# Optimization experiments

Hardware: AMD Instinct MI355X
Metric: run time of the kernel (lower is better)

The kernel has to match this reference:

```python
import jax, jax.numpy as jnp
import numpy as np

B, N = 4, 4096
CIN, COUT = 64, 64
K, R, BOX = 3, 32, 4
MLP = COUT * 4
HEADS = 4
EPS = 0.0


def setup_inputs() -> dict:
    key = jax.random.key(0)
    ks = jax.random.split(key, 16)
    s = lambda i, shape: jax.random.normal(ks[i], shape, jnp.float32) * 0.05
    return dict(
        features=jax.random.normal(ks[0], (B, CIN, N), jnp.float32),
        coords=jax.random.normal(ks[1], (B, 3, N), jnp.float32),
        conv_w=s(2, (COUT, CIN, K, K, K)), conv_b=jnp.zeros((COUT,), jnp.float32),
        ln1_g=jnp.ones((COUT,), jnp.float32), ln1_b=jnp.zeros((COUT,), jnp.float32),
        qkv_w=s(3, (3 * COUT, COUT)), qkv_b=jnp.zeros((3 * COUT,), jnp.float32),
        proj_w=s(4, (COUT, COUT)), proj_b=jnp.zeros((COUT,), jnp.float32),
        ln2_g=jnp.ones((COUT,), jnp.float32), ln2_b=jnp.zeros((COUT,), jnp.float32),
        mlp_w1=s(5, (MLP, COUT)), mlp_b1=jnp.zeros((MLP,), jnp.float32),
        mlp_w2=s(6, (COUT, MLP)), mlp_b2=jnp.zeros((COUT,), jnp.float32),
        se_w1=s(7, (COUT // 8, COUT)), se_w2=s(8, (COUT, COUT // 8)),
        pt_in_w=s(9, (COUT, CIN)), pt_in_b=jnp.zeros((COUT,), jnp.float32),
        q_w=s(10, (COUT // 4, COUT)), k_w=s(11, (COUT // 4, COUT)),
        v_w=s(12, (COUT, COUT)),
        trans_w=s(13, (COUT, COUT)), trans_b=jnp.zeros((COUT,), jnp.float32),
    )


def layernorm(x, g, b):
    m = x.mean(-1, keepdims=True)
    v = x.var(-1, keepdims=True)
    return (x - m) * jax.lax.rsqrt(v + 1e-5) * g + b


def voxelize(features, coords):
    # PVCNN-style: center, normalize to [0,1], scale to [0, R-1]; scatter-mean.
    c = coords - coords.mean(axis=2, keepdims=True)  # (B,3,N)
    mx = jnp.sqrt((c ** 2).sum(axis=1, keepdims=True)).max(axis=2, keepdims=True)
    nc = c / (2.0 * mx + EPS) + 0.5
    nc = jnp.clip(nc * R, 0.0, R - 1)  # float coords in [0, R-1]
    vc = jnp.round(nc).astype(jnp.int32)
    idx = (vc[:, 0] * R + vc[:, 1]) * R + vc[:, 2]
    idx = (idx + jnp.arange(B, dtype=jnp.int32)[:, None] * R ** 3).reshape(-1)
    flat = features.transpose(0, 2, 1).reshape(B * N, CIN)
    sums = jax.ops.segment_sum(flat, idx, num_segments=B * R ** 3)
    cnt = jax.ops.segment_sum(jnp.ones((B * N,), jnp.float32), idx, num_segments=B * R ** 3)
    avg = sums / jnp.maximum(cnt, 1.0)[:, None]
    grid = avg.reshape(B, R, R, R, CIN).transpose(0, 4, 1, 2, 3)  # (B,C,R,R,R)
    return grid, nc


def devoxelize(grid, nc):
    # trilinear gather from (B,C,R,R,R) at float coords nc (B,3,N)
    g = grid.reshape(B, COUT, R ** 3)
    x0 = jnp.floor(nc)
    f = nc - x0
    x0 = x0.astype(jnp.int32)
    out = jnp.zeros((B, COUT, N), jnp.float32)
    for dx in (0, 1):
        for dy in (0, 1):
            for dz in (0, 1):
                xi = jnp.clip(x0[:, 0] + dx, 0, R - 1)
                yi = jnp.clip(x0[:, 1] + dy, 0, R - 1)
                zi = jnp.clip(x0[:, 2] + dz, 0, R - 1)
                idx = (xi * R + yi) * R + zi  # (B,N)
                w = ((f[:, 0] if dx else 1 - f[:, 0]) *
                     (f[:, 1] if dy else 1 - f[:, 1]) *
                     (f[:, 2] if dz else 1 - f[:, 2]))
                vals = jnp.take_along_axis(g, jnp.broadcast_to(idx[:, None, :], (B, COUT, N)), axis=2)
                out = out + vals * w[:, None, :]
    return out


def voxel_encoder(grid, conv_w, conv_b, ln1_g, ln1_b, qkv_w, qkv_b, proj_w, proj_b,
                  ln2_g, ln2_b, mlp_w1, mlp_b1, mlp_w2, mlp_b2):
    x = jax.lax.conv_general_dilated(grid, conv_w, (1, 1, 1), 'SAME',
                                     dimension_numbers=('NCDHW', 'OIDHW', 'NCDHW'))
    x = jax.nn.relu(x + conv_b[None, :, None, None, None])
    nb = R // BOX
    # window partition -> (B*nb^3, BOX^3, C)
    t = x.transpose(0, 2, 3, 4, 1).reshape(B, nb, BOX, nb, BOX, nb, BOX, COUT)
    t = t.transpose(0, 1, 3, 5, 2, 4, 6, 7).reshape(B * nb ** 3, BOX ** 3, COUT)
    h = layernorm(t, ln1_g, ln1_b)
    qkv = h @ qkv_w.T + qkv_b
    q, k, v = jnp.split(qkv, 3, axis=-1)
    hd = COUT // HEADS
    sh = lambda z: z.reshape(z.shape[0], z.shape[1], HEADS, hd).transpose(0, 2, 1, 3)
    q, k, v = sh(q), sh(k), sh(v)
    attn = jax.nn.softmax(jnp.einsum('whid,whjd->whij', q, k) / np.float32(np.sqrt(hd)), axis=-1)
    o = jnp.einsum('whij,whjd->whid', attn, v).transpose(0, 2, 1, 3).reshape(t.shape)
    t = t + (o @ proj_w.T + proj_b)
    h = layernorm(t, ln2_g, ln2_b)
    t = t + (jax.nn.gelu(h @ mlp_w1.T + mlp_b1) @ mlp_w2.T + mlp_b2)
    t = t.reshape(B, nb, nb, nb, BOX, BOX, BOX, COUT)
    t = t.transpose(0, 1, 4, 2, 5, 3, 6, 7).reshape(B, R, R, R, COUT)
    return t.transpose(0, 4, 1, 2, 3)


def se3d(x, w1, w2):
    s = x.mean(axis=(2, 3, 4))  # (B,C)
    s = jax.nn.sigmoid(jax.nn.relu(s @ w1.T) @ w2.T)
    return x * s[:, :, None, None, None]


def point_branch(features, pt_in_w, pt_in_b, q_w, k_w, v_w, trans_w, trans_b):
    # PCT-style offset self-attention over points (shared transformer)
    x = jax.nn.relu(jnp.einsum('oc,bcn->bon', pt_in_w, features) + pt_in_b[None, :, None])
    q = jnp.einsum('dc,bcn->bdn', q_w, x)
    k = jnp.einsum('dc,bcn->bdn', k_w, x)
    v = jnp.einsum('oc,bcn->bon', v_w, x)
    attn = jax.nn.softmax(jnp.einsum('bdn,bdm->bnm', q, k) / np.float32(np.sqrt(q.shape[1])), axis=-1)
    o = jnp.einsum('bom,bnm->bon', v, attn)
    off = jax.nn.relu(jnp.einsum('oc,bcn->bon', trans_w, x - o) + trans_b[None, :, None])
    return x + off


def reference(features, coords, conv_w, conv_b, ln1_g, ln1_b, qkv_w, qkv_b, proj_w, proj_b,
              ln2_g, ln2_b, mlp_w1, mlp_b1, mlp_w2, mlp_b2, se_w1, se_w2,
              pt_in_w, pt_in_b, q_w, k_w, v_w, trans_w, trans_b):
    grid, nc = voxelize(features, coords)
    vf = voxel_encoder(grid, conv_w, conv_b, ln1_g, ln1_b, qkv_w, qkv_b, proj_w, proj_b,
                       ln2_g, ln2_b, mlp_w1, mlp_b1, mlp_w2, mlp_b2)
    vf = se3d(vf, se_w1, se_w2)
    vf = devoxelize(vf, nc)
    fused = vf + point_branch(features, pt_in_w, pt_in_b, q_w, k_w, v_w, trans_w, trans_b)
    return fused, coords
```

## Files before the change

kernel.cpp:

```cpp
#include <hip/hip_runtime.h>

#define BN 4
#define NP 4096
#define RV 32
#define VX (RV*RV*RV)

typedef __attribute__((ext_vector_type(8))) short bf16x8;
typedef __attribute__((ext_vector_type(4))) float f32x4;

__device__ __forceinline__ float bf2f(unsigned short u){
  union{unsigned u;float f;}v; v.u=((unsigned)u)<<16; return v.f; }
__device__ __forceinline__ unsigned short f2bf(float f){
  union{float f;unsigned u;}v; v.f=f; unsigned r=v.u + 0x7fffu + ((v.u>>16)&1u);
  return (unsigned short)(r>>16); }
__device__ __forceinline__ float2 bfp2f2(unsigned p){
  union{unsigned u;float f;}a,b; a.u=p<<16; b.u=p&0xffff0000u;
  float2 r; r.x=a.f; r.y=b.f; return r; }
__device__ __forceinline__ unsigned pack2bf(float a, float b){
  return (unsigned)f2bf(a) | ((unsigned)f2bf(b) << 16); }

union ABu { uint4 u; bf16x8 v; };

__global__ void stats_kernel(const float* __restrict__ coords, float* __restrict__ stats)
{
  __shared__ float red[256];
  __shared__ float mean[3];
  const int b = blockIdx.x;
  const int tid = threadIdx.x;
  float s0=0.f,s1=0.f,s2=0.f;
  for (int n = tid; n < NP; n += 256) {
    s0 += coords[((size_t)(b*3)+0)*NP + n];
    s1 += coords[((size_t)(b*3)+1)*NP + n];
    s2 += coords[((size_t)(b*3)+2)*NP + n];
  }
  float sv[3] = {s0,s1,s2};
  for (int ax = 0; ax < 3; ax++) {
    __syncthreads();
    red[tid] = sv[ax];
    __syncthreads();
    for (int st = 128; st > 0; st >>= 1) {
      if (tid < st) red[tid] += red[tid + st];
      __syncthreads();
    }
    if (tid == 0) mean[ax] = red[0] * (1.f / NP);
  }
  __syncthreads();
  float mx = 0.f;
  for (int n = tid; n < NP; n += 256) {
    float d0 = coords[((size_t)(b*3)+0)*NP + n] - mean[0];
    float d1 = coords[((size_t)(b*3)+1)*NP + n] - mean[1];
    float d2 = coords[((size_t)(b*3)+2)*NP + n] - mean[2];
    mx = fmaxf(mx, sqrtf(d0*d0 + d1*d1 + d2*d2));
  }
  __syncthreads();
  red[tid] = mx;
  __syncthreads();
  for (int st = 128; st > 0; st >>= 1) {
    if (tid < st) red[tid] = fmaxf(red[tid], red[tid + st]);
    __syncthreads();
  }
  if (tid == 0) {
    stats[b*4+0] = mean[0]; stats[b*4+1] = mean[1];
    stats[b*4+2] = mean[2]; stats[b*4+3] = red[0];
  }
}

__global__ void scatter_kernel(const float* __restrict__ features,
                               const float* __restrict__ coords,
                               const float* __restrict__ stats,
                               float* __restrict__ nc,
                               float* __restrict__ sums, float* __restrict__ cnt)
{
  int t = blockIdx.x*256 + threadIdx.x;
  int part = t & 3;
  int p = t >> 2;
  int b = p >> 12;
  int n = p & 4095;
  float m0 = stats[b*4+0], m1 = stats[b*4+1], m2 = stats[b*4+2], mx = stats[b*4+3];
  float inv = 1.f / (2.f * mx);
  float c0 = (coords[((size_t)(b*3)+0)*NP + n] - m0) * inv + 0.5f;
  float c1 = (coords[((size_t)(b*3)+1)*NP + n] - m1) * inv + 0.5f;
  float c2 = (coords[((size_t)(b*3)+2)*NP + n] - m2) * inv + 0.5f;
  float g0 = fminf(fmaxf(c0 * 32.f, 0.f), 31.f);
  float g1 = fminf(fmaxf(c1 * 32.f, 0.f), 31.f);
  float g2 = fminf(fmaxf(c2 * 32.f, 0.f), 31.f);
  int v0 = (int)rintf(g0), v1 = (int)rintf(g1), v2 = (int)rintf(g2);
  int idx = (v0*32 + v1)*32 + v2 + b*VX;
  if (part == 0) {
    nc[((size_t)(b*3)+0)*NP + n] = g0;
    nc[((size_t)(b*3)+1)*NP + n] = g1;
    nc[((size_t)(b*3)+2)*NP + n] = g2;
    atomicAdd(&cnt[idx], 1.f);
  }
  const float* fp = features + (size_t)(b*64)*NP + n;
  float* sp = sums + (size_t)idx*64;
  for (int i = part*16; i < part*16+16; i++)
    atomicAdd(&sp[i], fp[(size_t)i*NP]);
}

__global__ void wprep_kernel(const float* __restrict__ wt, unsigned short* __restrict__ wpre)
{
  int t = blockIdx.x*256 + threadIdx.x;
  if (t >= 27*64*8) return;
  int c16 = t & 7, o = (t >> 3) & 63, tap = t >> 9;
  size_t dst = ((size_t)(tap*64 + o)*8 + (c16 ^ (o & 7))) * 8;
  #pragma unroll
  for (int j = 0; j < 8; j++) {
    int i = c16*8 + j;
    wpre[dst + j] = f2bf(wt[(o*64 + i)*27 + tap]);
  }
}

__global__ void eprep_kernel(const float* __restrict__ qkv_w, const float* __restrict__ proj_w,
                             const float* __restrict__ w1, const float* __restrict__ w2,
                             const float* __restrict__ pt_in_w, const float* __restrict__ q_w,
                             const float* __restrict__ k_w, const float* __restrict__ v_w,
                             unsigned short* __restrict__ dst)
{
  int t = blockIdx.x*256 + threadIdx.x;
  if (t >= 59392) return;
  float v;
  if (t < 4096)       v = qkv_w[t] * 0.25f;
  else if (t < 12288) v = qkv_w[t];
  else if (t < 16384) v = proj_w[t-12288];
  else if (t < 32768) v = w1[t-16384];
  else if (t < 49152) v = w2[t-32768];
  else {
    int t2 = t - 49152;
    if (t2 < 4096)      v = pt_in_w[t2];
    else if (t2 < 5120) v = q_w[t2-4096] * 0.25f;
    else if (t2 < 6144) v = k_w[t2-5120];
    else                v = v_w[t2-6144];
  }
  dst[t] = f2bf(v);
}

__global__ __launch_bounds__(256) void conv_mfma_kernel(
    const float* __restrict__ sums, const float* __restrict__ cnt,
    const unsigned short* __restrict__ wpre,
    const float* __restrict__ bias, unsigned short* __restrict__ gout)
{
  __shared__ uint4 plane[6*34*8];
  __shared__ uint4 wsm[3*64*8];
  const int tid = threadIdx.x;
  const int blk = blockIdx.x;
  const int yq = blk & 7, z = (blk >> 3) & 31, b = blk >> 8;
  const int y0 = yq * 4;
  const int w  = tid >> 6;
  const int lm = tid & 15;
  const int kg = (tid >> 4) & 3;

  f32x4 acc[2][4];
  #pragma unroll
  for (int mt = 0; mt < 2; mt++)
    #pragma unroll
    for (int nt = 0; nt < 4; nt++)
      #pragma unroll
      for (int r = 0; r < 4; r++) acc[mt][nt][r] = 0.f;

  float bv[4];
  #pragma unroll
  for (int nt = 0; nt < 4; nt++) bv[nt] = bias[nt*16 + lm];

  for (int kd = 0; kd < 3; kd++) {
    const int zz = z + kd - 1;
    if (zz < 0 || zz >= 32) continue;
    __syncthreads();
    for (int e = tid; e < 6*34*8; e += 256) {
      int c16 = e & 7;
      int sx  = (e >> 3) % 34;
      int yl  = e / (34*8);
      int yy = y0 - 1 + yl, x = sx - 1;
      uint4 val = make_uint4(0u,0u,0u,0u);
      if (yy >= 0 && yy < 32 && x >= 0 && x < 32) {
        size_t vox = (size_t)(b*VX) + (zz*32 + yy)*32 + x;
        float rc = 1.f / fmaxf(cnt[vox], 1.f);
        const float* src = sums + vox*64 + c16*8;
        float4 f0 = *(const float4*)(src);
        float4 f1 = *(const float4*)(src + 4);
        val.x = pack2bf(f0.x*rc, f0.y*rc);
        val.y = pack2bf(f0.z*rc, f0.w*rc);
        val.z = pack2bf(f1.x*rc, f1.y*rc);
        val.w = pack2bf(f1.z*rc, f1.w*rc);
      }
      plane[(yl*34 + sx)*8 + (c16 ^ (sx & 7))] = val;
    }
    for (int kh = 0; kh < 3; kh++) {
      __syncthreads();
      const uint4* wsrc = (const uint4*)wpre + (size_t)((kd*3 + kh)*3)*512;
      for (int e = tid; e < 1536; e += 256) wsm[e] = wsrc[e];
      __syncthreads();
      const int yi = w + kh;
      #pragma unroll
      for (int kw = 0; kw < 3; kw++) {
        const int sxa = lm + kw, sxb = sxa + 16;
        const int swz = sxa & 7;
        #pragma unroll
        for (int ch = 0; ch < 2; ch++) {
          const int cb = ch*4 + kg;
          ABu a0, a1, w0, w1, w2, w3;
          a0.u = plane[(yi*34 + sxa)*8 + (cb ^ swz)];
          a1.u = plane[(yi*34 + sxb)*8 + (cb ^ swz)];
          const int wsz = cb ^ (lm & 7);
          w0.u = wsm[(kw*64 +      lm)*8 + wsz];
          w1.u = wsm[(kw*64 + 16 + lm)*8 + wsz];
          w2.u = wsm[(kw*64 + 32 + lm)*8 + wsz];
          w3.u = wsm[(kw*64 + 48 + lm)*8 + wsz];
          acc[0][0] = __builtin_amdgcn_mfma_f32_16x16x32_bf16(a0.v, w0.v, acc[0][0], 0,0,0);
          acc[1][0] = __builtin_amdgcn_mfma_f32_16x16x32_bf16(a1.v, w0.v, acc[1][0], 0,0,0);
          acc[0][1] = __builtin_amdgcn_mfma_f32_16x16x32_bf16(a0.v, w1.v, acc[0][1], 0,0,0);
          acc[1][1] = __builtin_amdgcn_mfma_f32_16x16x32_bf16(a1.v, w1.v, acc[1][1], 0,0,0);
          acc[0][2] = __builtin_amdgcn_mfma_f32_16x16x32_bf16(a0.v, w2.v, acc[0][2], 0,0,0);
          acc[1][2] = __builtin_amdgcn_mfma_f32_16x16x32_bf16(a1.v, w2.v, acc[1][2], 0,0,0);
          acc[0][3] = __builtin_amdgcn_mfma_f32_16x16x32_bf16(a0.v, w3.v, acc[0][3], 0,0,0);
          acc[1][3] = __builtin_amdgcn_mfma_f32_16x16x32_bf16(a1.v, w3.v, acc[1][3], 0,0,0);
        }
      }
    }
  }
  const int y = y0 + w;
  #pragma unroll
  for (int mt = 0; mt < 2; mt++) {
    #pragma unroll
    for (int r = 0; r < 4; r++) {
      const int x = mt*16 + kg*4 + r;
      unsigned short* dst = gout + ((size_t)(b*VX) + (z*32 + y)*32 + x)*64 + lm;
      #pragma unroll
      for (int nt = 0; nt < 4; nt++)
        dst[nt*16] = f2bf(fmaxf(acc[mt][nt][r] + bv[nt], 0.f));
    }
  }
}

__global__ __launch_bounds__(256) void encoder_kernel(
    unsigned short* __restrict__ grid,
    const float* __restrict__ ln1_g, const float* __restrict__ ln1_b,
    const float* __restrict__ qkv_b, const float* __restrict__ proj_b,
    const float* __restrict__ ln2_g, const float* __restrict__ ln2_b,
    const float* __restrict__ b1, const float* __restrict__ b2,
    const unsigned short* __restrict__ encw,
    float* __restrict__ se_sum)
{
  __shared__ unsigned short t_b[64*72];
  __shared__ unsigned short h_b[64*72];
  __shared__ unsigned short q_b[64*72];
  __shared__ unsigned short k_b[64*72];
  __shared__ unsigned short v_b[64*72];
  __shared__ float mean_s[64], rstd_s[64];
  __shared__ float scratch[1024];

  const unsigned short* wqb = encw;
  const unsigned short* wpb = encw + 12288;
  const unsigned short* w1b = encw + 16384;
  const unsigned short* w2b = encw + 32768;

  const int tid = threadIdx.x;
  const int w = tid >> 6;
  const int lane = tid & 63;
  const int cl = lane & 15;
  const int quad = lane >> 4;
  const int win = blockIdx.x;
  const int b = win >> 9, wn = win & 511;
  const int zb = wn >> 6, yb = (wn >> 3) & 7, xb = wn & 7;
  const size_t gb = (size_t)b * VX * 64;

  for (int e = tid; e < 512; e += 256) {
    int tok = e >> 3, cg8 = e & 7;
    int zl = tok >> 4, yl = (tok >> 2) & 3, xl = tok & 3;
    int vox = ((zb*4+zl)*32 + (yb*4+yl))*32 + (xb*4+xl);
    *(uint4*)(t_b + tok*72 + cg8*8) = *(const uint4*)(grid + gb + (size_t)vox*64 + cg8*8);
  }
  __syncthreads();
  {
    int i = tid >> 2, part = tid & 3;
    ABu r0, r1;
    r0.u = *(const uint4*)(t_b + i*72 + part*16);
    r1.u = *(const uint4*)(t_b + i*72 + part*16 + 8);
    float sum = 0.f, sq = 0.f;
    const unsigned* u0 = (const unsigned*)&r0;
    const unsigned* u1 = (const unsigned*)&r1;
    #pragma unroll
    for (int j = 0; j < 4; j++) {
      float2 a = bfp2f2(u0[j]); float2 c = bfp2f2(u1[j]);
      sum += a.x + a.y + c.x + c.y;
      sq  += a.x*a.x + a.y*a.y + c.x*c.x + c.y*c.y;
    }
    sum += __shfl_xor(sum, 1); sq += __shfl_xor(sq, 1);
    sum += __shfl_xor(sum, 2); sq += __shfl_xor(sq, 2);
    if (part == 0) {
      float m = sum * (1.f/64.f);
      float var = sq * (1.f/64.f) - m*m;
      mean_s[i] = m; rstd_s[i] = rsqrtf(var + 1e-5f);
    }
  }
  __syncthreads();
  {
    const int cg = tid & 15, tq = tid >> 4;
    float4 g4 = *(const float4*)(ln1_g + cg*4);
    float4 b4 = *(const float4*)(ln1_b + cg*4);
    #pragma unroll
    for (int k = 0; k < 4; k++) {
      int tok = tq + k*16;
      uint2 tv = *(const uint2*)(t_b + tok*72 + cg*4);
      float2 x01 = bfp2f2(tv.x), x23 = bfp2f2(tv.y);
      float m = mean_s[tok], r = rstd_s[tok];
      float h0 = (x01.x-m)*r*g4.x + b4.x;
      float h1 = (x01.y-m)*r*g4.y + b4.y;
      float h2 = (x23.x-m)*r*g4.z + b4.z;
      float h3 = (x23.y-m)*r*g4.w + b4.w;
      *(uint2*)(h_b + tok*72 + cg*4) = make_uint2(pack2bf(h0,h1), pack2bf(h2,h3));
    }
  }
  __syncthreads();
  {
    #pragma unroll
    for (int ci = 0; ci < 3; ci++) {
      const int d0 = 48*w + ci*16;
      ABu a0, a1;
      a0.u = *(const uint4*)(wqb + (d0 + cl)*64 + quad*8);
      a1.u = *(const uint4*)(wqb + (d0 + cl)*64 + 32 + quad*8);
      float4 bias4 = *(const float4*)(qkv_b + d0 + quad*4);
      if (d0 < 64) { bias4.x *= 0.25f; bias4.y *= 0.25f; bias4.z *= 0.25f; bias4.w *= 0.25f; }
      #pragma unroll
      for (int tt = 0; tt < 4; tt++) {
        ABu h0, h1;
        h0.u = *(const uint4*)(h_b + (tt*16 + cl)*72 + quad*8);
        h1.u = *(const uint4*)(h_b + (tt*16 + cl)*72 + 32 + quad*8);
        f32x4 d = {0.f,0.f,0.f,0.f};
        d = __builtin_amdgcn_mfma_f32_16x16x32_bf16(a0.v, h0.v, d, 0,0,0);
        d = __builtin_amdgcn_mfma_f32_16x16x32_bf16(a1.v, h1.v, d, 0,0,0);
        if (d0 < 64) {
          *(uint2*)(q_b + (tt*16+cl)*72 + d0 + quad*4) =
            make_uint2(pack2bf(d[0]+bias4.x, d[1]+bias4.y),
                       pack2bf(d[2]+bias4.z, d[3]+bias4.w));
        } else if (d0 < 128) {
          *(uint2*)(k_b + (tt*16+cl)*72 + (d0-64) + quad*4) =
            make_uint2(pack2bf(d[0]+bias4.x, d[1]+bias4.y),
                       pack2bf(d[2]+bias4.z, d[3]+bias4.w));
        } else {
          const float* bp = (const float*)&bias4;
          #pragma unroll
          for (int r = 0; r < 4; r++)
            v_b[((d0-128) + quad*4 + r)*72 + tt*16 + cl] = f2bf(d[r] + bp[r]);
        }
      }
    }
  }
  __syncthreads();
  uint2 pk[4];
  {
    const uint4 z4 = make_uint4(0u,0u,0u,0u);
    #pragma unroll
    for (int h = 0; h < 4; h++) {
      const int hb = h*16;
      ABu bq;
      if (quad < 2) bq.u = *(const uint4*)(q_b + (w*16 + cl)*72 + hb + quad*8);
      else bq.u = z4;
      float sc[4][4];
      #pragma unroll
      for (int tj = 0; tj < 4; tj++) {
        ABu ak;
        if (quad < 2) ak.u = *(const uint4*)(k_b + (tj*16 + cl)*72 + hb + quad*8);
        else ak.u = z4;
        f32x4 d = {0.f,0.f,0.f,0.f};
        d = __builtin_amdgcn_mfma_f32_16x16x32_bf16(ak.v, bq.v, d, 0,0,0);
        #pragma unroll
        for (int r = 0; r < 4; r++) sc[tj][r] = d[r];
      }
      float mx = -1e30f;
      #pragma unroll
      for (int tj = 0; tj < 4; tj++)
        #pragma unroll
        for (int r = 0; r < 4; r++) mx = fmaxf(mx, sc[tj][r]);
      mx = fmaxf(mx, __shfl_xor(mx, 16));
      mx = fmaxf(mx, __shfl_xor(mx, 32));
      float psum = 0.f;
      #pragma unroll
      for (int tj = 0; tj < 4; tj++) {
        float p0 = __expf(sc[tj][0]-mx), p1 = __expf(sc[tj][1]-mx);
        float p2 = __expf(sc[tj][2]-mx), p3 = __expf(sc[tj][3]-mx);
        psum += p0+p1+p2+p3;
        *(uint2*)(h_b + (w*16+cl)*72 + tj*16 + quad*4) =
            make_uint2(pack2bf(p0,p1), pack2bf(p2,p3));
      }
      psum += __shfl_xor(psum, 16);
      psum += __shfl_xor(psum, 32);
      float inv = 1.f / psum;
      f32x4 oacc = {0.f,0.f,0.f,0.f};
      #pragma unroll
      for (int kk = 0; kk < 2; kk++) {
        ABu av, bp;
        av.u = *(const uint4*)(v_b + (hb + cl)*72 + kk*32 + quad*8);
        bp.u = *(const uint4*)(h_b + (w*16 + cl)*72 + kk*32 + quad*8);
        oacc = __builtin_amdgcn_mfma_f32_16x16x32_bf16(av.v, bp.v, oacc, 0,0,0);
      }
      pk[h] = make_uint2(pack2bf(oacc[0]*inv, oacc[1]*inv),
                         pack2bf(oacc[2]*inv, oacc[3]*inv));
    }
  }
  __syncthreads();
  #pragma unroll
  for (int h = 0; h < 4; h++)
    *(uint2*)(k_b + (w*16+cl)*72 + h*16 + quad*4) = pk[h];
  __syncthreads();
  {
    const int c0 = w*16;
    ABu a0, a1;
    a0.u = *(const uint4*)(wpb + (c0 + cl)*64 + quad*8);
    a1.u = *(const uint4*)(wpb + (c0 + cl)*64 + 32 + quad*8);
    float4 pb4 = *(const float4*)(proj_b + c0 + quad*4);
    #pragma unroll
    for (int tt = 0; tt < 4; tt++) {
      ABu o0, o1;
      o0.u = *(const uint4*)(k_b + (tt*16 + cl)*72 + quad*8);
      o1.u = *(const uint4*)(k_b + (tt*16 + cl)*72 + 32 + quad*8);
      f32x4 d = {0.f,0.f,0.f,0.f};
      d = __builtin_amdgcn_mfma_f32_16x16x32_bf16(a0.v, o0.v, d, 0,0,0);
      d = __builtin_amdgcn_mfma_f32_16x16x32_bf16(a1.v, o1.v, d, 0,0,0);
      uint2* tp = (uint2*)(t_b + (tt*16+cl)*72 + c0 + quad*4);
      uint2 told = *tp;
      float2 t01 = bfp2f2(told.x), t23 = bfp2f2(told.y);
      float n0v = t01.x + d[0] + pb4.x;
      float n1v = t01.y + d[1] + pb4.y;
      float n2v = t23.x + d[2] + pb4.z;
      float n3v = t23.y + d[3] + pb4.w;
      *tp = make_uint2(pack2bf(n0v,n1v), pack2bf(n2v,n3v));
      float s = n0v+n1v+n2v+n3v;
      float qq = n0v*n0v + n1v*n1v + n2v*n2v + n3v*n3v;
      s  += __shfl_xor(s, 16);  s  += __shfl_xor(s, 32);
      qq += __shfl_xor(qq, 16); qq += __shfl_xor(qq, 32);
      if (quad == 0) {
        scratch[(tt*16+cl)*4 + w] = s;
        scratch[256 + (tt*16+cl)*4 + w] = qq;
      }
    }
  }
  __syncthreads();
  if (tid < 64) {
    float s  = scratch[tid*4] + scratch[tid*4+1] + scratch[tid*4+2] + scratch[tid*4+3];
    float qq = scratch[256+tid*4] + scratch[256+tid*4+1]
             + scratch[256+tid*4+2] + scratch[256+tid*4+3];
    float m = s * (1.f/64.f);
    float var = qq * (1.f/64.f) - m*m;
    mean_s[tid] = m; rstd_s[tid] = rsqrtf(var + 1e-5f);
  }
  __syncthreads();
  {
    const int cg = tid & 15, tq = tid >> 4;
    float4 g4 = *(const float4*)(ln2_g + cg*4);
    float4 b4 = *(const float4*)(ln2_b + cg*4);
    #pragma unroll
    for (int k = 0; k < 4; k++) {
      int tok = tq + k*16;
      uint2 tv = *(const uint2*)(t_b + tok*72 + cg*4);
      float2 x01 = bfp2f2(tv.x), x23 = bfp2f2(tv.y);
      float m = mean_s[tok], r = rstd_s[tok];
      float h0 = (x01.x-m)*r*g4.x + b4.x;
      float h1 = (x01.y-m)*r*g4.y + b4.y;
      float h2 = (x23.x-m)*r*g4.z + b4.z;
      float h3 = (x23.y-m)*r*g4.w + b4.w;
      *(uint2*)(h_b + tok*72 + cg*4) = make_uint2(pack2bf(h0,h1), pack2bf(h2,h3));
    }
  }
  __syncthreads();
  {
    const int c0 = w*16;
    ABu hb0[4], hb1[4];
    #pragma unroll
    for (int tt = 0; tt < 4; tt++) {
      hb0[tt].u = *(const uint4*)(h_b + (tt*16 + cl)*72 + quad*8);
      hb1[tt].u = *(const uint4*)(h_b + (tt*16 + cl)*72 + 32 + quad*8);
    }
    f32x4 acc2[4];
    #pragma unroll
    for (int tt = 0; tt < 4; tt++)
      #pragma unroll
      for (int r = 0; r < 4; r++) acc2[tt][r] = 0.f;
    for (int ch = 0; ch < 4; ch++) {
      const int m0 = ch*64 + w*16;
      ABu a0, a1;
      a0.u = *(const uint4*)(w1b + (m0 + cl)*64 + quad*8);
      a1.u = *(const uint4*)(w1b + (m0 + cl)*64 + 32 + quad*8);
      float4 b14 = *(const float4*)(b1 + m0 + quad*4);
      const float* bp = (const float*)&b14;
      #pragma unroll
      for (int tt = 0; tt < 4; tt++) {
        f32x4 d = {0.f,0.f,0.f,0.f};
        d = __builtin_amdgcn_mfma_f32_16x16x32_bf16(a0.v, hb0[tt].v, d, 0,0,0);
        d = __builtin_amdgcn_mfma_f32_16x16x32_bf16(a1.v, hb1[tt].v, d, 0,0,0);
        float g[4];
        #pragma unroll
        for (int r = 0; r < 4; r++) {
          float x = d[r] + bp[r];
          float u = 1.5957691f * (x + 0.044715f*x*x*x);
          g[r] = x / (1.f + __expf(-u));
        }
        *(uint2*)(q_b + (tt*16+cl)*72 + w*16 + quad*4) =
            make_uint2(pack2bf(g[0],g[1]), pack2bf(g[2],g[3]));
      }
      __syncthreads();
      ABu a20, a21;
      a20.u = *(const uint4*)(w2b + (c0 + cl)*256 + ch*64 + quad*8);
      a21.u = *(const uint4*)(w2b + (c0 + cl)*256 + ch*64 + 32 + quad*8);
      #pragma unroll
      for (int tt = 0; tt < 4; tt++) {
        ABu bh0, bh1;
        bh0.u = *(const uint4*)(q_b + (tt*16 + cl)*72 + quad*8);
        bh1.u = *(const uint4*)(q_b + (tt*16 + cl)*72 + 32 + quad*8);
        acc2[tt] = __builtin_amdgcn_mfma_f32_16x16x32_bf16(a20.v, bh0.v, acc2[tt], 0,0,0);
        acc2[tt] = __builtin_amdgcn_mfma_f32_16x16x32_bf16(a21.v, bh1.v, acc2[tt], 0,0,0);
      }
      __syncthreads();
    }
    float4 b24 = *(const float4*)(b2 + c0 + quad*4);
    #pragma unroll
    for (int tt = 0; tt < 4; tt++) {
      uint2* tp = (uint2*)(t_b + (tt*16+cl)*72 + c0 + quad*4);
      uint2 told = *tp;
      float2 t01 = bfp2f2(told.x), t23 = bfp2f2(told.y);
      *tp = make_uint2(pack2bf(t01.x + acc2[tt][0] + b24.x, t01.y + acc2[tt][1] + b24.y),
                       pack2bf(t23.x + acc2[tt][2] + b24.z, t23.y + acc2[tt][3] + b24.w));
    }
  }
  __syncthreads();
  for (int e = tid; e < 512; e += 256) {
    int tok = e >> 3, cg8 = e & 7;
    int zl = tok >> 4, yl = (tok >> 2) & 3, xl = tok & 3;
    int vox = ((zb*4+zl)*32 + (yb*4+yl))*32 + (xb*4+xl);
    *(uint4*)(grid + gb + (size_t)vox*64 + cg8*8) = *(const uint4*)(t_b + tok*72 + cg8*8);
  }
  {
    const int cg = tid & 15, tq = tid >> 4;
    float4 p = {0.f,0.f,0.f,0.f};
    #pragma unroll
    for (int k = 0; k < 4; k++) {
      int tok = tq + k*16;
      uint2 tv = *(const uint2*)(t_b + tok*72 + cg*4);
      float2 x01 = bfp2f2(tv.x), x23 = bfp2f2(tv.y);
      p.x += x01.x; p.y += x01.y; p.z += x23.x; p.w += x23.y;
    }
    ((float4*)scratch)[cg*16 + tq] = p;
  }
  __syncthreads();
  if (tid < 64) {
    int cg = tid >> 2, j = tid & 3;
    float s = 0.f;
    #pragma unroll
    for (int g = 0; g < 16; g++) s += scratch[(cg*16+g)*4 + j];
    atomicAdd(&se_sum[b*64 + tid], s);
  }
}

__global__ void se_kernel(const float* __restrict__ se_sum, const float* __restrict__ w1,
                          const float* __restrict__ w2, float* __restrict__ scale)
{
  __shared__ float mean_s[256];
  __shared__ float z1[32];
  int tid = threadIdx.x;
  mean_s[tid] = se_sum[tid] * (1.f / VX);
  __syncthreads();
  if (tid < 32) {
    int bb = tid >> 3, j = tid & 7;
    float a = 0.f;
    for (int c = 0; c < 64; c++) a += mean_s[bb*64 + c] * w1[j*64 + c];
    z1[tid] = fmaxf(a, 0.f);
  }
  __syncthreads();
  int b = tid >> 6, c = tid & 63;
  float a = 0.f;
  for (int j = 0; j < 8; j++) a += z1[b*8 + j] * w2[c*8 + j];
  scale[tid] = 1.f / (1.f + __expf(-a));
}

__global__ __launch_bounds__(256) void point_in_kernel(
    const float* __restrict__ features, const float* __restrict__ pt_in_b,
    const unsigned short* __restrict__ ptw,
    float* __restrict__ x_t, unsigned short* __restrict__ q_bf,
    unsigned short* __restrict__ k_bf, unsigned short* __restrict__ v_tt)
{
  __shared__ unsigned short f_b[64*72];
  __shared__ unsigned short x_b[64*72];
  const int tid = threadIdx.x;
  const int blk = blockIdx.x;
  const int b = blk >> 6;
  const int n0 = (blk & 63) * 64;
  const int w = tid >> 6;
  const int lane = tid & 63;
  const int cl = lane & 15;
  const int quad = lane >> 4;

  for (int e = tid; e < 4096; e += 256) {
    int c = e >> 6, nl = e & 63;
    f_b[nl*72 + c] = f2bf(features[((size_t)(b*64 + c))*NP + n0 + nl]);
  }
  __syncthreads();
  const int m0 = w*16;
  {
    ABu a0, a1;
    a0.u = *(const uint4*)(ptw + (m0 + cl)*64 + quad*8);
    a1.u = *(const uint4*)(ptw + (m0 + cl)*64 + 32 + quad*8);
    float4 bi = *(const float4*)(pt_in_b + m0 + quad*4);
    #pragma unroll
    for (int tt = 0; tt < 4; tt++) {
      ABu f0, f1;
      f0.u = *(const uint4*)(f_b + (tt*16 + cl)*72 + quad*8);
      f1.u = *(const uint4*)(f_b + (tt*16 + cl)*72 + 32 + quad*8);
      f32x4 d = {0.f,0.f,0.f,0.f};
      d = __builtin_amdgcn_mfma_f32_16x16x32_bf16(a0.v, f0.v, d, 0,0,0);
      d = __builtin_amdgcn_mfma_f32_16x16x32_bf16(a1.v, f1.v, d, 0,0,0);
      float x0 = fmaxf(d[0]+bi.x, 0.f), x1 = fmaxf(d[1]+bi.y, 0.f);
      float x2 = fmaxf(d[2]+bi.z, 0.f), x3 = fmaxf(d[3]+bi.w, 0.f);
      const int n = tt*16 + cl;
      *(float4*)&x_t[((size_t)(b*NP) + n0 + n)*64 + m0 + quad*4] =
          make_float4(x0, x1, x2, x3);
      *(uint2*)(x_b + n*72 + m0 + quad*4) = make_uint2(pack2bf(x0,x1), pack2bf(x2,x3));
    }
  }
  __syncthreads();
  {
    const unsigned short* vwb = ptw + 6144;
    ABu a0, a1;
    a0.u = *(const uint4*)(vwb + (m0 + cl)*64 + quad*8);
    a1.u = *(const uint4*)(vwb + (m0 + cl)*64 + 32 + quad*8);
    #pragma unroll
    for (int tt = 0; tt < 4; tt++) {
      ABu x0, x1;
      x0.u = *(const uint4*)(x_b + (tt*16 + cl)*72 + quad*8);
      x1.u = *(const uint4*)(x_b + (tt*16 + cl)*72 + 32 + quad*8);
      f32x4 d = {0.f,0.f,0.f,0.f};
      d = __builtin_amdgcn_mfma_f32_16x16x32_bf16(a0.v, x0.v, d, 0,0,0);
      d = __builtin_amdgcn_mfma_f32_16x16x32_bf16(a1.v, x1.v, d, 0,0,0);
      const int n = n0 + tt*16 + cl;
      #pragma unroll
      for (int r = 0; r < 4; r++)
        v_tt[((size_t)(b*64) + m0 + quad*4 + r)*NP + n] = f2bf(d[r]);
    }
  }
  {
    const int which = w & 1, half = w >> 1;
    const unsigned short* wp = ptw + (which ? 5120 : 4096);
    unsigned short* dst = which ? k_bf : q_bf;
    ABu a0, a1;
    a0.u = *(const uint4*)(wp + cl*64 + quad*8);
    a1.u = *(const uint4*)(wp + cl*64 + 32 + quad*8);
    #pragma unroll
    for (int th = 0; th < 2; th++) {
      const int tt = half*2 + th;
      ABu x0, x1;
      x0.u = *(const uint4*)(x_b + (tt*16 + cl)*72 + quad*8);
      x1.u = *(const uint4*)(x_b + (tt*16 + cl)*72 + 32 + quad*8);
      f32x4 d = {0.f,0.f,0.f,0.f};
      d = __builtin_amdgcn_mfma_f32_16x16x32_bf16(a0.v, x0.v, d, 0,0,0);
      d = __builtin_amdgcn_mfma_f32_16x16x32_bf16(a1.v, x1.v, d, 0,0,0);
      const int n = tt*16 + cl;
      *(uint2*)(dst + ((size_t)(b*NP) + n0 + n)*16 + quad*4) =
          make_uint2(pack2bf(d[0],d[1]), pack2bf(d[2],d[3]));
    }
  }
}

__global__ __launch_bounds__(256) void point_attn_kernel(
    const unsigned short* __restrict__ q_bf, const unsigned short* __restrict__ k_bf,
    const unsigned short* __restrict__ v_tt,
    float* __restrict__ opart, float2* __restrict__ mlbuf)
{
  __shared__ unsigned short q_s[64*24];
  __shared__ unsigned short k_sh[2][64*24];
  __shared__ unsigned short v_sh[2][64*72];
  __shared__ unsigned short p_s[64*72];
  const int tid = threadIdx.x;
  const int blk = blockIdx.x;
  const int b = blk >> 8;
  const int nb = (blk >> 2) & 63;
  const int s = blk & 3;
  const int n0 = nb * 64;
  const int t_beg = s*16, t_end = s*16 + 16;
  const int w = tid >> 6;
  const int lane = tid & 63;
  const int cl = lane & 15;
  const int quad = lane >> 4;
  const uint4 z4 = make_uint4(0u,0u,0u,0u);

  const unsigned* qbu = (const unsigned*)q_bf;
  const unsigned* kbu = (const unsigned*)k_bf;
  const unsigned* vtu = (const unsigned*)v_tt;
  unsigned* q_su = (unsigned*)q_s;

  {
    unsigned* kd = (unsigned*)k_sh[0];
    unsigned* vd = (unsigned*)v_sh[0];
    for (int e = tid; e < 512; e += 256) {
      int tok = e >> 3, du = e & 7;
      q_su[tok*12 + du] = qbu[((size_t)(b*NP) + n0 + tok)*8 + du];
      kd[tok*12 + du]   = kbu[((size_t)(b*NP) + t_beg*64 + tok)*8 + du];
    }
    for (int e = tid; e < 2048; e += 256) {
      int cc = e >> 5, tu = e & 31;
      vd[cc*36 + tu] = vtu[((size_t)(b*64) + cc)*2048 + t_beg*32 + tu];
    }
  }
  float m_run = -1e30f, l_run = 0.f;
  f32x4 acc[4];
  #pragma unroll
  for (int ct = 0; ct < 4; ct++)
    #pragma unroll
    for (int r = 0; r < 4; r++) acc[ct][r] = 0.f;
  __syncthreads();

  ABu bq;
  if (quad < 2) bq.u = *(const uint4*)(q_s + (w*16 + cl)*24 + quad*8);
  else bq.u = z4;

  for (int t = t_beg; t < t_end; t++) {
    const int cur = t & 1;
    unsigned pk[2], pv[8];
    if (t+1 < t_end) {
      const int m1 = (t+1)*64;
      #pragma unroll
      for (int i = 0; i < 2; i++) {
        int e = tid + i*256;
        pk[i] = kbu[((size_t)(b*NP) + m1 + (e>>3))*8 + (e&7)];
      }
      #pragma unroll
      for (int i = 0; i < 8; i++) {
        int e = tid + i*256;
        pv[i] = vtu[((size_t)(b*64) + (e>>5))*2048 + (m1>>1) + (e&31)];
      }
    }
    const unsigned short* ks = k_sh[cur];
    const unsigned short* vs = v_sh[cur];
    float sc[4][4];
    #pragma unroll
    for (int tj = 0; tj < 4; tj++) {
      ABu ak;
      if (quad < 2) ak.u = *(const uint4*)(ks + (tj*16 + cl)*24 + quad*8);
      else ak.u = z4;
      f32x4 d = {0.f,0.f,0.f,0.f};
      d = __builtin_amdgcn_mfma_f32_16x16x32_bf16(ak.v, bq.v, d, 0,0,0);
      #pragma unroll
      for (int r = 0; r < 4; r++) sc[tj][r] = d[r];
    }
    float tmax = -1e30f;
    #pragma unroll
    for (int tj = 0; tj < 4; tj++)
      #pragma unroll
      for (int r = 0; r < 4; r++) tmax = fmaxf(tmax, sc[tj][r]);
    tmax = fmaxf(tmax, __shfl_xor(tmax, 16));
    tmax = fmaxf(tmax, __shfl_xor(tmax, 32));
    float mnew = fmaxf(m_run, tmax);
    float alpha = __expf(m_run - mnew);
    float psum = 0.f;
    #pragma unroll
    for (int tj = 0; tj < 4; tj++) {
      float p0 = __expf(sc[tj][0]-mnew), p1 = __expf(sc[tj][1]-mnew);
      float p2 = __expf(sc[tj][2]-mnew), p3 = __expf(sc[tj][3]-mnew);
      psum += p0+p1+p2+p3;
      *(uint2*)(p_s + (w*16+cl)*72 + tj*16 + quad*4) =
          make_uint2(pack2bf(p0,p1), pack2bf(p2,p3));
    }
    psum += __shfl_xor(psum, 16);
    psum += __shfl_xor(psum, 32);
    l_run = l_run*alpha + psum;
    m_run = mnew;
    #pragma unroll
    for (int ct = 0; ct < 4; ct++)
      #pragma unroll
      for (int r = 0; r < 4; r++) acc[ct][r] *= alpha;
    #pragma unroll
    for (int kk = 0; kk < 2; kk++) {
      ABu bp;
      bp.u = *(const uint4*)(p_s + (w*16 + cl)*72 + kk*32 + quad*8);
      #pragma unroll
      for (int ct = 0; ct < 4; ct++) {
        ABu av;
        av.u = *(const uint4*)(vs + (ct*16 + cl)*72 + kk*32 + quad*8);
        acc[ct] = __builtin_amdgcn_mfma_f32_16x16x32_bf16(av.v, bp.v, acc[ct], 0,0,0);
      }
    }
    __syncthreads();
    if (t+1 < t_end) {
      unsigned* kd = (unsigned*)k_sh[1-cur];
      unsigned* vd = (unsigned*)v_sh[1-cur];
      #pragma unroll
      for (int i = 0; i < 2; i++) {
        int e = tid + i*256;
        kd[(e>>3)*12 + (e&7)] = pk[i];
      }
      #pragma unroll
      for (int i = 0; i < 8; i++) {
        int e = tid + i*256;
        vd[(e>>5)*36 + (e&31)] = pv[i];
      }
    }
    __syncthreads();
  }
  const int tok = n0 + w*16 + cl;
  #pragma unroll
  for (int ct = 0; ct < 4; ct++) {
    float4 o4;
    o4.x = acc[ct][0]; o4.y = acc[ct][1]; o4.z = acc[ct][2]; o4.w = acc[ct][3];
    *(float4*)&opart[(((size_t)(s*BN + b))*NP + tok)*64 + ct*16 + quad*4] = o4;
  }
  if (quad == 0)
    mlbuf[(size_t)(s*BN + b)*NP + tok] = make_float2(m_run, l_run);
}

__global__ __launch_bounds__(256) void fuse_kernel(
    const float* __restrict__ x_t, const float* __restrict__ opart,
    const float2* __restrict__ mlbuf,
    const float* __restrict__ trans_w, const float* __restrict__ trans_b,
    const unsigned short* __restrict__ grid, const float* __restrict__ se_scale,
    const float* __restrict__ nc, float* __restrict__ out)
{
  __shared__ float tw_s[64*65];
  __shared__ float d_s[32*65];
  __shared__ float r_s[64*33];
  __shared__ float mw[32][6];
  const int tid = threadIdx.x;
  const int blk = blockIdx.x;
  const int b = blk >> 7;
  const int n0 = (blk & 127) * 32;
  for (int e = tid; e < 4096; e += 256) {
    int c = e >> 6, k = e & 63;
    tw_s[c*65 + k] = trans_w[e];
  }
  if (tid < 32) {
    int nl = tid;
    float m[4], l[4];
    #pragma unroll
    for (int s = 0; s < 4; s++) {
      float2 v = mlbuf[(size_t)(s*BN + b)*NP + n0 + nl];
      m[s] = v.x; l[s] = v.y;
    }
    float M = fmaxf(fmaxf(m[0], m[1]), fmaxf(m[2], m[3]));
    float L = 0.f;
    #pragma unroll
    for (int s = 0; s < 4; s++) {
      float ws = __expf(m[s] - M);
      mw[nl][s] = ws;
      L += l[s] * ws;
    }
    mw[nl][4] = 1.f / L;
  }
  __syncthreads();
  for (int e = tid; e < 2048; e += 256) {
    int nl = e >> 6, c = e & 63;
    size_t pbase = ((size_t)(b*NP) + n0 + nl)*64 + c;
    const size_t sstr = (size_t)BN*NP*64;
    float o = opart[pbase]        * mw[nl][0] + opart[pbase +   sstr] * mw[nl][1]
            + opart[pbase+2*sstr] * mw[nl][2] + opart[pbase + 3*sstr] * mw[nl][3];
    o *= mw[nl][4];
    d_s[nl*65 + c] = x_t[pbase] - o;
  }
  __syncthreads();
  const int cl = tid & 63, g = tid >> 6;
  const float ses = se_scale[b*64 + cl];
  const float tb = trans_b[cl];
  for (int t = 0; t < 8; t++) {
    int nl = g*8 + t;
    int n = n0 + nl;
    float off = 0.f;
    for (int k = 0; k < 64; k++) off += tw_s[cl*65 + k] * d_s[nl*65 + k];
    off = fmaxf(off + tb, 0.f);
    float ncx = nc[((size_t)(b*3)+0)*NP + n];
    float ncy = nc[((size_t)(b*3)+1)*NP + n];
    float ncz = nc[((size_t)(b*3)+2)*NP + n];
    float fx0 = floorf(ncx), fy0 = floorf(ncy), fz0 = floorf(ncz);
    int x0 = (int)fx0, y0 = (int)fy0, z0 = (int)fz0;
    float fx = ncx - fx0, fy = ncy - fy0, fz = ncz - fz0;
    float wx[2] = {1.f-fx, fx}, wy[2] = {1.f-fy, fy}, wz[2] = {1.f-fz, fz};
    float vf = 0.f;
    #pragma unroll
    for (int cor = 0; cor < 8; cor++) {
      int dx = cor >> 2, dy = (cor >> 1) & 1, dz = cor & 1;
      int xi = min(x0+dx, 31), yi = min(y0+dy, 31), zi = min(z0+dz, 31);
      float wgt = wx[dx]*wy[dy]*wz[dz];
      vf += wgt * bf2f(grid[((size_t)(b*VX) + (xi*32+yi)*32 + zi)*64 + cl]);
    }
    vf *= ses;
    float xval = x_t[((size_t)(b*NP) + n)*64 + cl];
    r_s[cl*33 + nl] = xval + off + vf;
  }
  __syncthreads();
  for (int e = tid; e < 2048; e += 256) {
    int c = e >> 5, nl = e & 31;
    out[((size_t)(b*64) + c)*NP + n0 + nl] = r_s[c*33 + nl];
  }
}

extern "C" void kernel_launch(void* const* d_in, const int* in_sizes, int n_in,
                              void* d_out, int out_size, void* d_ws, size_t ws_size,
                              hipStream_t stream)
{
  const float* features = (const float*)d_in[0];
  const float* coords   = (const float*)d_in[1];
  const float* conv_w   = (const float*)d_in[2];
  const float* conv_b   = (const float*)d_in[3];
  const float* ln1_g    = (const float*)d_in[4];
  const float* ln1_b    = (const float*)d_in[5];
  const float* qkv_w    = (const float*)d_in[6];
  const float* qkv_b    = (const float*)d_in[7];
  const float* proj_w   = (const float*)d_in[8];
  const float* proj_b   = (const float*)d_in[9];
  const float* ln2_g    = (const float*)d_in[10];
  const float* ln2_b    = (const float*)d_in[11];
  const float* mlp_w1   = (const float*)d_in[12];
  const float* mlp_b1   = (const float*)d_in[13];
  const float* mlp_w2   = (const float*)d_in[14];
  const float* mlp_b2   = (const float*)d_in[15];
  const float* se_w1    = (const float*)d_in[16];
  const float* se_w2    = (const float*)d_in[17];
  const float* pt_in_w  = (const float*)d_in[18];
  const float* pt_in_b  = (const float*)d_in[19];
  const float* q_w      = (const float*)d_in[20];
  const float* k_w      = (const float*)d_in[21];
  const float* v_w      = (const float*)d_in[22];
  const float* v_trans_w= (const float*)d_in[23];
  const float* v_trans_b= (const float*)d_in[24];

  char* ws = (char*)d_ws;
  float* stats    = (float*)(ws + 0);
  float* se_sum   = (float*)(ws + 256);
  float* se_scale = (float*)(ws + 1280);
  float* nc       = (float*)(ws + 4096);
  float* cnt      = (float*)(ws + 200704);
  float* grid0    = (float*)(ws + 724992);
  unsigned short* grid1b = (unsigned short*)(ws + 34279424);
  float* x_t = (float*)(ws + 724992);
  unsigned short* q_bf = (unsigned short*)(ws + 724992 + 4194304);
  unsigned short* k_bf = (unsigned short*)(ws + 724992 + 5242880);
  unsigned short* v_tt = (unsigned short*)(ws + 724992 + 6291456);
  float*  opart = (float*)(ws + 724992 + 10485760);
  float2* mlbuf = (float2*)(ws + 724992 + 27787264);
  unsigned short* wpre = (unsigned short*)d_out;
  unsigned short* encw = (unsigned short*)((char*)d_out + 221184);

  hipMemsetAsync(se_sum, 0, 1024, stream);
  hipMemsetAsync(cnt, 0, 524288 + 33554432, stream);

  wprep_kernel<<<54, 256, 0, stream>>>(conv_w, wpre);
  eprep_kernel<<<232, 256, 0, stream>>>(qkv_w, proj_w, mlp_w1, mlp_w2,
      pt_in_w, q_w, k_w, v_w, encw);
  stats_kernel<<<BN, 256, 0, stream>>>(coords, stats);
  scatter_kernel<<<256, 256, 0, stream>>>(features, coords, stats, nc, grid0, cnt);
  conv_mfma_kernel<<<1024, 256, 0, stream>>>(grid0, cnt, wpre, conv_b, grid1b);
  encoder_kernel<<<2048, 256, 0, stream>>>(grid1b, ln1_g, ln1_b, qkv_b, proj_b,
      ln2_g, ln2_b, mlp_b1, mlp_b2, encw, se_sum);
  se_kernel<<<1, 256, 0, stream>>>(se_sum, se_w1, se_w2, se_scale);
  point_in_kernel<<<256, 256, 0, stream>>>(features, pt_in_b, encw + 49152,
      x_t, q_bf, k_bf, v_tt);
  point_attn_kernel<<<1024, 256, 0, stream>>>(q_bf, k_bf, v_tt, opart, mlbuf);
  fuse_kernel<<<512, 256, 0, stream>>>(x_t, opart, mlbuf, v_trans_w, v_trans_b,
      grid1b, se_scale, nc, (float*)d_out);
  hipMemcpyAsync((char*)d_out + (size_t)BN*64*NP*4, coords, (size_t)BN*3*NP*4,
                 hipMemcpyDeviceToDevice, stream);
}
```

Baseline: 398.3 us.

## Replace vectorized LayerNorm and SE-reduction paths with scalar per-element loops in encoder

Simplifies the encoder kernel's elementwise stages. Grid load/store moves from 16-byte to 8-byte accesses, and the LayerNorm statistics and normalization loops now handle one bf16 element per thread instead of packed vectors. The fused LN2-statistics computation inside the projection epilogue is dropped in favour of a separate recompute pass over shared memory. The SE channel-sum reduction is rewritten with a smaller scratch buffer. This shrinks shared memory, but it adds more scalar LDS traffic, narrower global accesses and an extra pass.

```diff
diff --git a/kernel.cpp b/kernel.cpp
--- a/kernel.cpp
+++ b/kernel.cpp
@@ -247,7 +247,7 @@
   __shared__ unsigned short k_b[64*72];
   __shared__ unsigned short v_b[64*72];
   __shared__ float mean_s[64], rstd_s[64];
-  __shared__ float scratch[1024];
+  __shared__ float sered[256];
 
   const unsigned short* wqb = encw;
   const unsigned short* wpb = encw + 12288;
@@ -264,27 +264,17 @@
   const int zb = wn >> 6, yb = (wn >> 3) & 7, xb = wn & 7;
   const size_t gb = (size_t)b * VX * 64;
 
-  for (int e = tid; e < 512; e += 256) {
-    int tok = e >> 3, cg8 = e & 7;
+  for (int e = tid; e < 1024; e += 256) {
+    int tok = e >> 4, cg = e & 15;
     int zl = tok >> 4, yl = (tok >> 2) & 3, xl = tok & 3;
     int vox = ((zb*4+zl)*32 + (yb*4+yl))*32 + (xb*4+xl);
-    *(uint4*)(t_b + tok*72 + cg8*8) = *(const uint4*)(grid + gb + (size_t)vox*64 + cg8*8);
+    *(uint2*)(t_b + tok*72 + cg*4) = *(const uint2*)(grid + gb + (size_t)vox*64 + cg*4);
   }
   __syncthreads();
   {
     int i = tid >> 2, part = tid & 3;
-    ABu r0, r1;
-    r0.u = *(const uint4*)(t_b + i*72 + part*16);
-    r1.u = *(const uint4*)(t_b + i*72 + part*16 + 8);
     float sum = 0.f, sq = 0.f;
-    const unsigned* u0 = (const unsigned*)&r0;
-    const unsigned* u1 = (const unsigned*)&r1;
-    #pragma unroll
-    for (int j = 0; j < 4; j++) {
-      float2 a = bfp2f2(u0[j]); float2 c = bfp2f2(u1[j]);
-      sum += a.x + a.y + c.x + c.y;
-      sq  += a.x*a.x + a.y*a.y + c.x*c.x + c.y*c.y;
-    }
+    for (int c = part; c < 64; c += 4) { float x = bf2f(t_b[i*72+c]); sum += x; sq += x*x; }
     sum += __shfl_xor(sum, 1); sq += __shfl_xor(sq, 1);
     sum += __shfl_xor(sum, 2); sq += __shfl_xor(sq, 2);
     if (part == 0) {
@@ -294,22 +284,10 @@
     }
   }
   __syncthreads();
-  {
-    const int cg = tid & 15, tq = tid >> 4;
-    float4 g4 = *(const float4*)(ln1_g + cg*4);
-    float4 b4 = *(const float4*)(ln1_b + cg*4);
-    #pragma unroll
-    for (int k = 0; k < 4; k++) {
-      int tok = tq + k*16;
-      uint2 tv = *(const uint2*)(t_b + tok*72 + cg*4);
-      float2 x01 = bfp2f2(tv.x), x23 = bfp2f2(tv.y);
-      float m = mean_s[tok], r = rstd_s[tok];
-      float h0 = (x01.x-m)*r*g4.x + b4.x;
-      float h1 = (x01.y-m)*r*g4.y + b4.y;
-      float h2 = (x23.x-m)*r*g4.z + b4.z;
-      float h3 = (x23.y-m)*r*g4.w + b4.w;
-      *(uint2*)(h_b + tok*72 + cg*4) = make_uint2(pack2bf(h0,h1), pack2bf(h2,h3));
-    }
+  for (int e = tid; e < 4096; e += 256) {
+    int tok = e >> 6, c = e & 63;
+    float h = (bf2f(t_b[tok*72+c]) - mean_s[tok]) * rstd_s[tok] * ln1_g[c] + ln1_b[c];
+    h_b[tok*72 + c] = f2bf(h);
   }
   __syncthreads();
   {
@@ -420,47 +398,28 @@
       uint2* tp = (uint2*)(t_b + (tt*16+cl)*72 + c0 + quad*4);
       uint2 told = *tp;
       float2 t01 = bfp2f2(told.x), t23 = bfp2f2(told.y);
-      float n0v = t01.x + d[0] + pb4.x;
-      float n1v = t01.y + d[1] + pb4.y;
-      float n2v = t23.x + d[2] + pb4.z;
-      float n3v = t23.y + d[3] + pb4.w;
-      *tp = make_uint2(pack2bf(n0v,n1v), pack2bf(n2v,n3v));
-      float s = n0v+n1v+n2v+n3v;
-      float qq = n0v*n0v + n1v*n1v + n2v*n2v + n3v*n3v;
-      s  += __shfl_xor(s, 16);  s  += __shfl_xor(s, 32);
-      qq += __shfl_xor(qq, 16); qq += __shfl_xor(qq, 32);
-      if (quad == 0) {
-        scratch[(tt*16+cl)*4 + w] = s;
-        scratch[256 + (tt*16+cl)*4 + w] = qq;
-      }
-    }
-  }
-  __syncthreads();
-  if (tid < 64) {
-    float s  = scratch[tid*4] + scratch[tid*4+1] + scratch[tid*4+2] + scratch[tid*4+3];
-    float qq = scratch[256+tid*4] + scratch[256+tid*4+1]
-             + scratch[256+tid*4+2] + scratch[256+tid*4+3];
-    float m = s * (1.f/64.f);
-    float var = qq * (1.f/64.f) - m*m;
-    mean_s[tid] = m; rstd_s[tid] = rsqrtf(var + 1e-5f);
-  }
-  __syncthreads();
-  {
-    const int cg = tid & 15, tq = tid >> 4;
-    float4 g4 = *(const float4*)(ln2_g + cg*4);
-    float4 b4 = *(const float4*)(ln2_b + cg*4);
-    #pragma unroll
-    for (int k = 0; k < 4; k++) {
-      int tok = tq + k*16;
-      uint2 tv = *(const uint2*)(t_b + tok*72 + cg*4);
-      float2 x01 = bfp2f2(tv.x), x23 = bfp2f2(tv.y);
-      float m = mean_s[tok], r = rstd_s[tok];
-      float h0 = (x01.x-m)*r*g4.x + b4.x;
-      float h1 = (x01.y-m)*r*g4.y + b4.y;
-      float h2 = (x23.x-m)*r*g4.z + b4.z;
-      float h3 = (x23.y-m)*r*g4.w + b4.w;
-      *(uint2*)(h_b + tok*72 + cg*4) = make_uint2(pack2bf(h0,h1), pack2bf(h2,h3));
-    }
+      *tp = make_uint2(pack2bf(t01.x + d[0] + pb4.x, t01.y + d[1] + pb4.y),
+                       pack2bf(t23.x + d[2] + pb4.z, t23.y + d[3] + pb4.w));
+    }
+  }
+  __syncthreads();
+  {
+    int i = tid >> 2, part = tid & 3;
+    float sum = 0.f, sq = 0.f;
+    for (int c = part; c < 64; c += 4) { float x = bf2f(t_b[i*72+c]); sum += x; sq += x*x; }
+    sum += __shfl_xor(sum, 1); sq += __shfl_xor(sq, 1);
+    sum += __shfl_xor(sum, 2); sq += __shfl_xor(sq, 2);
+    if (part == 0) {
+      float m = sum * (1.f/64.f);
+      float var = sq * (1.f/64.f) - m*m;
+      mean_s[i] = m; rstd_s[i] = rsqrtf(var + 1e-5f);
+    }
+  }
+  __syncthreads();
+  for (int e = tid; e < 4096; e += 256) {
+    int tok = e >> 6, c = e & 63;
+    float h = (bf2f(t_b[tok*72+c]) - mean_s[tok]) * rstd_s[tok] * ln2_g[c] + ln2_b[c];
+    h_b[tok*72 + c] = f2bf(h);
   }
   __syncthreads();
   {
@@ -523,32 +482,23 @@
     }
   }
   __syncthreads();
-  for (int e = tid; e < 512; e += 256) {
-    int tok = e >> 3, cg8 = e & 7;
+  for (int e = tid; e < 1024; e += 256) {
+    int tok = e >> 4, cg = e & 15;
     int zl = tok >> 4, yl = (tok >> 2) & 3, xl = tok & 3;
     int vox = ((zb*4+zl)*32 + (yb*4+yl))*32 + (xb*4+xl);
-    *(uint4*)(grid + gb + (size_t)vox*64 + cg8*8) = *(const uint4*)(t_b + tok*72 + cg8*8);
-  }
-  {
-    const int cg = tid & 15, tq = tid >> 4;
-    float4 p = {0.f,0.f,0.f,0.f};
-    #pragma unroll
-    for (int k = 0; k < 4; k++) {
-      int tok = tq + k*16;
-      uint2 tv = *(const uint2*)(t_b + tok*72 + cg*4);
-      float2 x01 = bfp2f2(tv.x), x23 = bfp2f2(tv.y);
-      p.x += x01.x; p.y += x01.y; p.z += x23.x; p.w += x23.y;
-    }
-    ((float4*)scratch)[cg*16 + tq] = p;
-  }
-  __syncthreads();
-  if (tid < 64) {
-    int cg = tid >> 2, j = tid & 3;
-    float s = 0.f;
-    #pragma unroll
-    for (int g = 0; g < 16; g++) s += scratch[(cg*16+g)*4 + j];
-    atomicAdd(&se_sum[b*64 + tid], s);
-  }
+    *(uint2*)(grid + gb + (size_t)vox*64 + cg*4) = *(const uint2*)(t_b + tok*72 + cg*4);
+  }
+  {
+    int c = tid & 63, quarter = tid >> 6;
+    float ps = 0.f;
+    #pragma unroll
+    for (int t = 0; t < 16; t++) ps += bf2f(t_b[(quarter*16+t)*72 + c]);
+    sered[quarter*64 + c] = ps;
+  }
+  __syncthreads();
+  if (tid < 64)
+    atomicAdd(&se_sum[b*64 + tid],
+              sered[tid] + sered[64+tid] + sered[128+tid] + sered[192+tid]);
 }
 
 __global__ void se_kernel(const float* __restrict__ se_sum, const float* __restrict__ w1,
```

After: 406.6 us, median of 2. 1.02x slower.
